# Kernel optimization log

Hardware: AMD Instinct MI355X
Metric: run time of the kernel (lower is better)

## Reference

```python
import jax, jax.numpy as jnp
import numpy as np

D_IN = 512
HLS = [1024, 1024, 512]
N_Q = 4096
N_K = 16384
N_CLASSES = 100
BN_EPS = 1e-5


def _bn(x, gamma, beta):
    # BatchNorm1d in training mode: per-batch mean/biased-var normalization
    m = jnp.mean(x, axis=0)
    v = jnp.var(x, axis=0)
    return gamma * (x - m) * jax.lax.rsqrt(v + BN_EPS) + beta


def _neg_cdist(a, b):
    # -||a_i - b_j||_2 via expanded form (GEMM-dominated)
    a2 = jnp.sum(a * a, axis=1, keepdims=True)          # [N,1]
    b2 = jnp.sum(b * b, axis=1, keepdims=True).T        # [1,M]
    d2 = a2 + b2 - 2.0 * (a @ b.T)                      # [N,M]
    return -jnp.sqrt(jnp.maximum(d2, 0.0))


def setup_inputs() -> dict:
    key = jax.random.key(0)
    ks = jax.random.split(key, 32)
    inp = {
        "x": jax.random.normal(ks[0], (N_Q, D_IN), jnp.float32),
        "x_n": jax.random.normal(ks[1], (N_K, D_IN), jnp.float32),
        "y_n": jax.random.randint(ks[2], (N_K,), 0, N_CLASSES, jnp.int32),
        "in_gamma": jnp.ones((D_IN,), jnp.float32),
        "in_beta": jnp.zeros((D_IN,), jnp.float32),
    }
    dims = [D_IN] + HLS
    ki = 3
    for i in range(len(HLS)):
        fan_in = dims[i]
        bound = 1.0 / np.sqrt(fan_in)
        inp[f"W{i}"] = jax.random.uniform(ks[ki], (dims[i + 1], dims[i]), jnp.float32, -bound, bound); ki += 1
        inp[f"b{i}"] = jax.random.uniform(ks[ki], (dims[i + 1],), jnp.float32, -bound, bound); ki += 1
        inp[f"g{i}"] = jnp.ones((dims[i + 1],), jnp.float32)
        inp[f"bt{i}"] = jnp.zeros((dims[i + 1],), jnp.float32)
    return inp


def reference(x, x_n, y_n, in_gamma, in_beta,
              W0, b0, g0, bt0, W1, b1, g1, bt1, W2, b2, g2, bt2):
    x = _bn(x, in_gamma, in_beta)
    x_n = _bn(x_n, in_gamma, in_beta)
    layers = [(W0, b0, g0, bt0), (W1, b1, g1, bt1), (W2, b2, g2, bt2)]
    for W, b, g, bt in layers:
        x = _bn(jnp.tanh(x @ W.T + b), g, bt)
        x_n = _bn(jnp.tanh(x_n @ W.T + b), g, bt)
    sim = _neg_cdist(x, x_n)                       # [N_Q, N_K]
    scores = jax.nn.softmax(sim, axis=1)
    y_ohe = jax.nn.one_hot(y_n, N_CLASSES, dtype=x.dtype)  # [N_K, C]
    return jnp.clip(scores @ y_ohe, 0.0, 1.0)
```

## Files before the change

### kernel.cpp

```cpp
#include <hip/hip_runtime.h>
#include <math.h>

#define NQ 4096
#define NK 16384
#define NROWS 20480
#define NCLS 100
#define PCLS 112
#define DCH 16

typedef __attribute__((ext_vector_type(8))) short bf16x8;
typedef __attribute__((ext_vector_type(4))) float f32x4;

__device__ inline unsigned short f2bf(float f) {
  unsigned u = __float_as_uint(f);
  u += 0x7fff + ((u >> 16) & 1);
  return (unsigned short)(u >> 16);
}
__device__ inline void upk(unsigned u, float& a, float& b) {
  a = __uint_as_float(u << 16);
  b = __uint_as_float(u & 0xffff0000u);
}
__device__ inline float fast_tanh(float x) {
  float e = __expf(2.f * x);
  return 1.f - 2.f / (e + 1.f);
}
__device__ inline void gload_lds16(const unsigned short* g, unsigned short* l) {
  __builtin_amdgcn_global_load_lds(
      (const __attribute__((address_space(1))) unsigned int*)g,
      (__attribute__((address_space(3))) unsigned int*)l, 16, 0, 0);
}

__global__ __launch_bounds__(256) void conv2_bf16(
    const float* __restrict__ x, const float* __restrict__ xn,
    unsigned short* __restrict__ outp) {
  const size_t n4q = (size_t)NQ * 512 / 4;
  const size_t n4 = (size_t)NROWS * 512 / 4;
  size_t i = (size_t)blockIdx.x * 256 + threadIdx.x;
  size_t stride = (size_t)gridDim.x * 256;
  for (; i < n4; i += stride) {
    float4 v = (i < n4q) ? ((const float4*)x)[i] : ((const float4*)xn)[i - n4q];
    unsigned lo = (unsigned)f2bf(v.x) | ((unsigned)f2bf(v.y) << 16);
    unsigned hi = (unsigned)f2bf(v.z) | ((unsigned)f2bf(v.w) << 16);
    ((uint2*)outp)[i] = make_uint2(lo, hi);
  }
}

__global__ __launch_bounds__(256) void colstats2(
    const float* __restrict__ x, const float* __restrict__ xn,
    float* __restrict__ part) {
  int j = blockIdx.x * 256 + threadIdx.x;
  int c = blockIdx.y;
  int seg = blockIdx.z;
  const float* A = seg ? xn : x;
  int rpc = seg ? (NK / 64) : (NQ / 64);
  float* p4 = part + (size_t)seg * 64 * 2 * 512;
  const float* p = A + (size_t)c * rpc * 512 + j;
  float s = 0.f, s2 = 0.f;
#pragma unroll 4
  for (int r = 0; r < rpc; ++r) {
    float v = p[(size_t)r * 512];
    s += v; s2 += v * v;
  }
  p4[(size_t)c * 2 * 512 + j] = s;
  p4[(size_t)c * 2 * 512 + 512 + j] = s2;
}

__global__ __launch_bounds__(256) void finish_ab2(
    const float* __restrict__ part,
    const float* __restrict__ g, const float* __restrict__ bt,
    float* __restrict__ abq, float* __restrict__ abk) {
  int j = blockIdx.x * 256 + threadIdx.x;
  int seg = blockIdx.y;
  const float* p4 = part + (size_t)seg * 64 * 2 * 512;
  float invN = seg ? (1.0f / NK) : (1.0f / NQ);
  float* ab = seg ? abk : abq;
  float s = 0.f, s2 = 0.f;
  for (int c = 0; c < 64; ++c) {
    s += p4[(size_t)c * 2 * 512 + j];
    s2 += p4[(size_t)c * 2 * 512 + 512 + j];
  }
  float m = s * invN;
  float v = fmaxf(s2 * invN - m * m, 0.f);
  float a = g[j] * rsqrtf(v + 1e-5f);
  ab[2 * j] = a;
  ab[2 * j + 1] = bt[j] - a * m;
}

__global__ __launch_bounds__(256) void ab_from_stats2(
    const float* __restrict__ stq, const float* __restrict__ stk,
    const float* __restrict__ g, const float* __restrict__ bt,
    float* __restrict__ abq, float* __restrict__ abk, int M) {
  int j = blockIdx.x * 256 + threadIdx.x;
  if (j >= M) return;
  int seg = blockIdx.y;
  const float* st = seg ? stk : stq;
  float invN = seg ? (1.0f / NK) : (1.0f / NQ);
  float* ab = seg ? abk : abq;
  float s = st[2 * j], s2 = st[2 * j + 1];
  float m = s * invN;
  float v = fmaxf(s2 * invN - m * m, 0.f);
  float a = g[j] * rsqrtf(v + 1e-5f);
  ab[2 * j] = a;
  ab[2 * j + 1] = bt[j] - a * m;
}

__global__ __launch_bounds__(256) void fold_w2(
    const float* __restrict__ W, const float* __restrict__ b,
    const float* __restrict__ abq, const float* __restrict__ abk, int K,
    unsigned short* __restrict__ Woq, unsigned short* __restrict__ Wok,
    float* __restrict__ boq, float* __restrict__ bok,
    float* __restrict__ statq, float* __restrict__ statk, int M) {
  int j = blockIdx.x;
  int t = threadIdx.x;
  if (j == 0) for (int i = t; i < 2 * M; i += 256) statq[i] = 0.f;
  if (j == 1) for (int i = t; i < 2 * M; i += 256) statk[i] = 0.f;
  const float* Wr = W + (size_t)j * K;
  unsigned short* Wq = Woq + (size_t)j * K;
  unsigned short* Wk = Wok + (size_t)j * K;
  float sq = 0.f, sk = 0.f;
  for (int k = t; k < K; k += 256) {
    float w = Wr[k];
    Wq[k] = f2bf(abq[2 * k] * w);
    Wk[k] = f2bf(abk[2 * k] * w);
    sq += abq[2 * k + 1] * w;
    sk += abk[2 * k + 1] * w;
  }
  __shared__ float redq[4], redk[4];
#pragma unroll
  for (int off = 32; off; off >>= 1) {
    sq += __shfl_down(sq, off, 64);
    sk += __shfl_down(sk, off, 64);
  }
  if ((t & 63) == 0) { redq[t >> 6] = sq; redk[t >> 6] = sk; }
  __syncthreads();
  if (t == 0) {
    boq[j] = b[j] + redq[0] + redq[1] + redq[2] + redq[3];
    bok[j] = b[j] + redk[0] + redk[1] + redk[2] + redk[3];
  }
}

__global__ __launch_bounds__(256) void gemm_v8(
    const unsigned short* __restrict__ A,
    const unsigned short* __restrict__ Wq, const unsigned short* __restrict__ Wk,
    const float* __restrict__ bq, const float* __restrict__ bk,
    unsigned short* __restrict__ C,
    float* __restrict__ stq, float* __restrict__ stk, int M, int K) {
  __shared__ unsigned short As[4][128 * 32];
  __shared__ unsigned short Ws[4][128 * 32];
  int tid = threadIdx.x;
  int l = tid & 63, w = tid >> 6;
  int rowBase = blockIdx.y * 128, colBase = blockIdx.x * 128;
  int seg = rowBase >= NQ;
  const unsigned short* W = seg ? Wk : Wq;
  const float* bias = seg ? bk : bq;
  float* st = seg ? stk : stq;
  int rowOff = (w >> 1) * 64, colOff = (w & 1) * 64;
  int fr = l & 15, fc = l >> 4;

  const unsigned short* Ag[2];
  const unsigned short* Wg[2];
  int slot[2];
#pragma unroll
  for (int j = 0; j < 2; ++j) {
    int i = tid + j * 256;
    int r = i >> 2, c = (i & 3) ^ (r & 3);
    slot[j] = i * 8;
    Ag[j] = A + (size_t)(rowBase + r) * K + c * 8;
    Wg[j] = W + (size_t)(colBase + r) * K + c * 8;
  }
  auto stage = [&](int s, int bb) {
    int ko = s * 32;
#pragma unroll
    for (int j = 0; j < 2; ++j) {
      gload_lds16(Ag[j] + ko, &As[bb][0] + slot[j]);
      gload_lds16(Wg[j] + ko, &Ws[bb][0] + slot[j]);
    }
  };

  f32x4 acc[4][4];
#pragma unroll
  for (int m = 0; m < 4; ++m)
#pragma unroll
    for (int n = 0; n < 4; ++n) acc[m][n] = (f32x4){0.f, 0.f, 0.f, 0.f};

  int NS = K >> 5;
  stage(0, 0);
  stage(1, 1);
  stage(2, 2);
  for (int s = 0; s < NS; ++s) {
    if (s + 2 < NS) {
      asm volatile("s_waitcnt vmcnt(8)" ::: "memory");
    } else if (s + 1 < NS) {
      asm volatile("s_waitcnt vmcnt(4)" ::: "memory");
    } else {
      asm volatile("s_waitcnt vmcnt(0)" ::: "memory");
    }
    __builtin_amdgcn_s_barrier();
    __builtin_amdgcn_sched_barrier(0);
    int b = s & 3;
    bf16x8 av[4], bv[4];
#pragma unroll
    for (int m = 0; m < 4; ++m) {
      int row = rowOff + m * 16 + fr;
      int p = fc ^ (row & 3);
      av[m] = *(const bf16x8*)((const char*)&As[b][0] + row * 64 + p * 16);
    }
#pragma unroll
    for (int n = 0; n < 4; ++n) {
      int row = colOff + n * 16 + fr;
      int p = fc ^ (row & 3);
      bv[n] = *(const bf16x8*)((const char*)&Ws[b][0] + row * 64 + p * 16);
    }
    if (s + 3 < NS) stage(s + 3, (s + 3) & 3);
#pragma unroll
    for (int m = 0; m < 4; ++m)
#pragma unroll
      for (int n = 0; n < 4; ++n)
        acc[m][n] = __builtin_amdgcn_mfma_f32_16x16x32_bf16(av[m], bv[n], acc[m][n], 0, 0, 0);
  }

  float ts1[4] = {0.f, 0.f, 0.f, 0.f};
  float ts2[4] = {0.f, 0.f, 0.f, 0.f};
#pragma unroll
  for (int m = 0; m < 4; ++m) {
#pragma unroll
    for (int r = 0; r < 4; ++r) {
      size_t row = rowBase + rowOff + m * 16 + fc * 4 + r;
      unsigned short* Crow = C + row * M;
#pragma unroll
      for (int n = 0; n < 4; ++n) {
        int col = colBase + colOff + n * 16 + fr;
        float val = fast_tanh(acc[m][n][r] + bias[col]);
        Crow[col] = f2bf(val);
        ts1[n] += val;
        ts2[n] += val * val;
      }
    }
  }
#pragma unroll
  for (int n = 0; n < 4; ++n) {
    float s1 = ts1[n], s2 = ts2[n];
    s1 += __shfl_xor(s1, 16, 64); s1 += __shfl_xor(s1, 32, 64);
    s2 += __shfl_xor(s2, 16, 64); s2 += __shfl_xor(s2, 32, 64);
    if (fc == 0) {
      int col = colBase + colOff + n * 16 + fr;
      atomicAdd(&st[2 * col], s1);
      atomicAdd(&st[2 * col + 1], s2);
    }
  }
}

__global__ __launch_bounds__(256) void bn_final2(
    unsigned short* __restrict__ F, const float* __restrict__ abq,
    const float* __restrict__ abk, float* __restrict__ norms) {
  int w = threadIdx.x >> 6, l = threadIdx.x & 63;
  int row = blockIdx.x * 4 + w;
  const float* ab = (row < NQ) ? abq : abk;
  unsigned short* p = F + (size_t)row * 512 + l * 8;
  uint4 v = *(const uint4*)p;
  int j0 = l * 8;
  float f[8];
  upk(v.x, f[0], f[1]); upk(v.y, f[2], f[3]);
  upk(v.z, f[4], f[5]); upk(v.w, f[6], f[7]);
  float s = 0.f;
  unsigned pk[4];
#pragma unroll
  for (int e = 0; e < 8; e += 2) {
    float a0 = ab[2 * (j0 + e)] * f[e] + ab[2 * (j0 + e) + 1];
    float a1 = ab[2 * (j0 + e + 1)] * f[e + 1] + ab[2 * (j0 + e + 1) + 1];
    s += a0 * a0 + a1 * a1;
    pk[e >> 1] = (unsigned)f2bf(a0) | ((unsigned)f2bf(a1) << 16);
  }
  *(uint4*)p = make_uint4(pk[0], pk[1], pk[2], pk[3]);
#pragma unroll
  for (int off = 32; off; off >>= 1) s += __shfl_down(s, off, 64);
  if (l == 0) norms[row] = s;
}

__global__ __launch_bounds__(256) void scatter_ohe(
    const int* __restrict__ yn, unsigned short* __restrict__ oheT) {
  int k = blockIdx.x * 256 + threadIdx.x;
  if (k < NK) oheT[(size_t)yn[k] * NK + k] = 0x3F80;
}

__global__ __launch_bounds__(512, 2) void dist_v5(
    const unsigned short* __restrict__ F,
    const float* __restrict__ norms,
    const unsigned short* __restrict__ oheT,
    float* __restrict__ part) {
  __shared__ unsigned short kbuf[3][128 * 64];
  __shared__ unsigned short Qs[8 * 64 * 64];
  __shared__ unsigned short Ps[64][136];
  __shared__ float k2s[1024];
  int tid = threadIdx.x;
  int l = tid & 63, w = tid >> 6;
  int qBase = blockIdx.x * 64;
  int kBase0 = blockIdx.y * 1024;
  int mg = w & 1, ng = w >> 1;
  int qtw = w & 3, cth = w >> 2;
  int fr = l & 15, fc = l >> 4;

  for (int i = tid; i < 1024; i += 512) k2s[i] = norms[NQ + kBase0 + i];
  float q2r0 = norms[qBase + mg * 32 + fr];
  float q2r1 = norms[qBase + mg * 32 + 16 + fr];
  __builtin_amdgcn_sched_barrier(0);

#pragma unroll
  for (int j = 0; j < 8; ++j) {
    int i = tid + j * 512;
    int ss = i >> 9;
    int row = (i >> 3) & 63;
    int c = (i & 7) ^ (row & 7);
    gload_lds16(F + (size_t)(qBase + row) * 512 + ss * 64 + c * 8, Qs + i * 8);
  }

  int i0 = tid, i1 = tid + 512;
  int r0 = i0 >> 3, c0 = (i0 & 7) ^ (r0 & 7);
  int r1 = i1 >> 3, c1 = (i1 & 7) ^ (r1 & 7);
  auto stage = [&](int slice, int bb) {
    int kRow = kBase0 + (slice >> 3) * 128;
    int ko = (slice & 7) * 64;
    gload_lds16(F + (size_t)(NQ + kRow + r0) * 512 + ko + c0 * 8,
                &kbuf[bb][0] + i0 * 8);
    gload_lds16(F + (size_t)(NQ + kRow + r1) * 512 + ko + c1 * 8,
                &kbuf[bb][0] + i1 * 8);
  };

  f32x4 accC[4];
#pragma unroll
  for (int c = 0; c < 4; ++c) accC[c] = (f32x4){0.f, 0.f, 0.f, 0.f};

  stage(0, 0);
  stage(1, 1);
  asm volatile("s_waitcnt lgkmcnt(0)" ::: "memory");

  for (int kt = 0; kt < 8; ++kt) {
    f32x4 acc[2][2];
#pragma unroll
    for (int t2 = 0; t2 < 2; ++t2)
#pragma unroll
      for (int qt = 0; qt < 2; ++qt) acc[t2][qt] = (f32x4){0.f, 0.f, 0.f, 0.f};
    bf16x8 ob[4][4];
#pragma unroll
    for (int kc = 0; kc < 4; ++kc)
#pragma unroll
      for (int c = 0; c < 4; ++c) ob[kc][c] = (bf16x8){0, 0, 0, 0, 0, 0, 0, 0};
#pragma unroll
    for (int s = 0; s < 8; ++s) {
      int slice = kt * 8 + s;
      if (slice == 63) {
        asm volatile("s_waitcnt vmcnt(0)" ::: "memory");
      } else if (s == 1 || s == 2) {
        asm volatile("s_waitcnt vmcnt(18)" ::: "memory");
      } else {
        asm volatile("s_waitcnt vmcnt(2)" ::: "memory");
      }
      __builtin_amdgcn_s_barrier();
      __builtin_amdgcn_sched_barrier(0);
      int b = slice % 3;
      bf16x8 kv[2][2];
#pragma unroll
      for (int kc = 0; kc < 2; ++kc)
#pragma unroll
        for (int t2 = 0; t2 < 2; ++t2) {
          int row = ng * 32 + t2 * 16 + fr;
          int sl = (kc * 4 + fc) ^ (row & 7);
          kv[kc][t2] = *(const bf16x8*)((const char*)&kbuf[b][0] + row * 128 + sl * 16);
        }
      bf16x8 avx[2][2];
#pragma unroll
      for (int kc = 0; kc < 2; ++kc)
#pragma unroll
        for (int qt = 0; qt < 2; ++qt) {
          int row = mg * 32 + qt * 16 + fr;
          int sl = (kc * 4 + fc) ^ (fr & 7);
          avx[kc][qt] = *(const bf16x8*)((const char*)Qs + s * 8192 + row * 128 + sl * 16);
        }
      if (slice + 2 < 64) stage(slice + 2, (slice + 2) % 3);
      if (s == 0) {
        __builtin_amdgcn_sched_barrier(0);
#pragma unroll
        for (int kc = 0; kc < 4; ++kc)
#pragma unroll
          for (int c = 0; c < 4; ++c) {
            int ctg = cth * 4 + c;
            if (ctg < 7)
              ob[kc][c] = *(const bf16x8*)(
                  oheT + (size_t)(ctg * 16 + fr) * NK + kBase0 + kt * 128 + kc * 32 + fc * 8);
          }
        __builtin_amdgcn_sched_barrier(0);
      }
#pragma unroll
      for (int kc = 0; kc < 2; ++kc)
#pragma unroll
        for (int t2 = 0; t2 < 2; ++t2)
#pragma unroll
          for (int qt = 0; qt < 2; ++qt)
            acc[t2][qt] = __builtin_amdgcn_mfma_f32_16x16x32_bf16(
                kv[kc][t2], avx[kc][qt], acc[t2][qt], 0, 0, 0);
    }
#pragma unroll
    for (int t2 = 0; t2 < 2; ++t2) {
      float k2v[4];
#pragma unroll
      for (int r = 0; r < 4; ++r)
        k2v[r] = k2s[kt * 128 + ng * 32 + t2 * 16 + fc * 4 + r];
#pragma unroll
      for (int qt = 0; qt < 2; ++qt) {
        int q = mg * 32 + qt * 16 + fr;
        float q2 = qt ? q2r1 : q2r0;
        float pv[4];
#pragma unroll
        for (int r = 0; r < 4; ++r) {
          float d2 = q2 + k2v[r] - 2.f * acc[t2][qt][r];
          pv[r] = __expf(-sqrtf(fmaxf(d2, 0.f)));
        }
        unsigned lo = (unsigned)f2bf(pv[0]) | ((unsigned)f2bf(pv[1]) << 16);
        unsigned hi = (unsigned)f2bf(pv[2]) | ((unsigned)f2bf(pv[3]) << 16);
        *(uint2*)(&Ps[q][ng * 32 + t2 * 16 + fc * 4]) = make_uint2(lo, hi);
      }
    }
    asm volatile("s_waitcnt lgkmcnt(0)" ::: "memory");
    __builtin_amdgcn_s_barrier();
    __builtin_amdgcn_sched_barrier(0);
#pragma unroll
    for (int kc = 0; kc < 4; ++kc) {
      bf16x8 pa = *(const bf16x8*)(&Ps[qtw * 16 + fr][kc * 32 + fc * 8]);
#pragma unroll
      for (int c = 0; c < 4; ++c) {
        int ctg = cth * 4 + c;
        if (ctg < 7)
          accC[c] = __builtin_amdgcn_mfma_f32_16x16x32_bf16(pa, ob[kc][c], accC[c], 0, 0, 0);
      }
    }
  }
#pragma unroll
  for (int c = 0; c < 4; ++c) {
    int ctg = cth * 4 + c;
    if (ctg < 7) {
#pragma unroll
      for (int r = 0; r < 4; ++r) {
        int q = qBase + qtw * 16 + fc * 4 + r;
        part[((size_t)q * DCH + blockIdx.y) * PCLS + ctg * 16 + fr] = accC[c][r];
      }
    }
  }
}

__global__ __launch_bounds__(128) void combine_out(
    const float* __restrict__ part, float* __restrict__ outp) {
  int q = blockIdx.x;
  int t = threadIdx.x;
  float num = 0.f;
  if (t < NCLS) {
#pragma unroll
    for (int ch = 0; ch < DCH; ++ch)
      num += part[((size_t)q * DCH + ch) * PCLS + t];
  }
  __shared__ float sn[128];
  sn[t] = (t < NCLS) ? num : 0.f;
  __syncthreads();
#pragma unroll
  for (int off = 64; off; off >>= 1) {
    if (t < off) sn[t] += sn[t + off];
    __syncthreads();
  }
  float L = sn[0];
  if (t < NCLS) outp[(size_t)q * NCLS + t] = fminf(fmaxf(num / L, 0.f), 1.f);
}

extern "C" void kernel_launch(void* const* d_in, const int* in_sizes, int n_in,
                              void* d_out, int out_size, void* d_ws, size_t ws_size,
                              hipStream_t stream) {
  (void)in_sizes; (void)n_in; (void)out_size; (void)ws_size;
  const float* x   = (const float*)d_in[0];
  const float* xn  = (const float*)d_in[1];
  const int*   yn  = (const int*)d_in[2];
  const float* ing = (const float*)d_in[3];
  const float* inb = (const float*)d_in[4];
  const float* Wl[3]  = {(const float*)d_in[5], (const float*)d_in[9],  (const float*)d_in[13]};
  const float* bl[3]  = {(const float*)d_in[6], (const float*)d_in[10], (const float*)d_in[14]};
  const float* gl[3]  = {(const float*)d_in[7], (const float*)d_in[11], (const float*)d_in[15]};
  const float* btl[3] = {(const float*)d_in[8], (const float*)d_in[12], (const float*)d_in[16]};
  float* outp = (float*)d_out;

  unsigned short* featA = (unsigned short*)d_ws;
  unsigned short* featB = featA + (size_t)NROWS * 1024;
  unsigned short* wq  = featB + (size_t)NROWS * 1024;
  unsigned short* wk  = wq + (size_t)1024 * 1024;
  unsigned short* ohe = wk + (size_t)1024 * 1024;
  float* spart = (float*)(ohe + (size_t)PCLS * NK);
  float* abq   = spart + 2 * 64 * 2 * 512;
  float* abk   = abq + 2048;
  float* statq = abk + 2048;
  float* statk = statq + 2048;
  float* bpq   = statk + 2048;
  float* bpk   = bpq + 1024;
  float* norms = bpk + 1024;
  float* part  = norms + NROWS;

  colstats2<<<dim3(2, 64, 2), 256, 0, stream>>>(x, xn, spart);
  finish_ab2<<<dim3(2, 2), 256, 0, stream>>>(spart, ing, inb, abq, abk);

  conv2_bf16<<<2048, 256, 0, stream>>>(x, xn, featA);

  hipMemsetAsync(ohe, 0, (size_t)PCLS * NK * sizeof(unsigned short), stream);
  scatter_ohe<<<NK / 256, 256, 0, stream>>>(yn, ohe);

  int dims[4] = {512, 1024, 1024, 512};
  unsigned short *src = featA, *dst = featB;
  for (int lyr = 0; lyr < 3; ++lyr) {
    int K = dims[lyr], M = dims[lyr + 1];
    fold_w2<<<M, 256, 0, stream>>>(Wl[lyr], bl[lyr], abq, abk, K,
                                   wq, wk, bpq, bpk, statq, statk, M);
    gemm_v8<<<dim3(M / 128, NROWS / 128), 256, 0, stream>>>(
        src, wq, wk, bpq, bpk, dst, statq, statk, M, K);
    ab_from_stats2<<<dim3((M + 255) / 256, 2), 256, 0, stream>>>(
        statq, statk, gl[lyr], btl[lyr], abq, abk, M);
    unsigned short* t = src; src = dst; dst = t;
  }
  bn_final2<<<NROWS / 4, 256, 0, stream>>>(src, abq, abk, norms);

  dist_v5<<<dim3(NQ / 64, DCH), 512, 0, stream>>>(src, norms, ohe, part);
  combine_out<<<NQ, 128, 0, stream>>>(part, outp);
}
```

Measured before the change: 503.7 us.

## Load key tiles directly from global memory into registers, dropping LDS triple buffer

The distance kernel no longer stages key-feature slices through a triple-buffered shared-memory ring with async global-to-LDS loads and per-slice barriers. Each wave now reads its key fragments straight from global memory into registers, and the one-hot class tiles are loaded unconditionally at the start of each key tile, with the class index clamped. This removes per-slice barriers and frees LDS, which may allow higher occupancy. In exchange, the global loads are uncoalesced and duplicated across the waves that share a key tile, and the loads are not software-pipelined, so memory latency may be exposed.

```diff
diff --git a/kernel.cpp b/kernel.cpp
--- a/kernel.cpp
+++ b/kernel.cpp
@@ -283,12 +283,11 @@
   if (k < NK) oheT[(size_t)yn[k] * NK + k] = 0x3F80;
 }
 
-__global__ __launch_bounds__(512, 2) void dist_v5(
+__global__ __launch_bounds__(512, 2) void dist_v10(
     const unsigned short* __restrict__ F,
     const float* __restrict__ norms,
     const unsigned short* __restrict__ oheT,
     float* __restrict__ part) {
-  __shared__ unsigned short kbuf[3][128 * 64];
   __shared__ unsigned short Qs[8 * 64 * 64];
   __shared__ unsigned short Ps[64][136];
   __shared__ float k2s[1024];
@@ -303,7 +302,6 @@
   for (int i = tid; i < 1024; i += 512) k2s[i] = norms[NQ + kBase0 + i];
   float q2r0 = norms[qBase + mg * 32 + fr];
   float q2r1 = norms[qBase + mg * 32 + 16 + fr];
-  __builtin_amdgcn_sched_barrier(0);
 
 #pragma unroll
   for (int j = 0; j < 8; ++j) {
@@ -313,26 +311,12 @@
     int c = (i & 7) ^ (row & 7);
     gload_lds16(F + (size_t)(qBase + row) * 512 + ss * 64 + c * 8, Qs + i * 8);
   }
-
-  int i0 = tid, i1 = tid + 512;
-  int r0 = i0 >> 3, c0 = (i0 & 7) ^ (r0 & 7);
-  int r1 = i1 >> 3, c1 = (i1 & 7) ^ (r1 & 7);
-  auto stage = [&](int slice, int bb) {
-    int kRow = kBase0 + (slice >> 3) * 128;
-    int ko = (slice & 7) * 64;
-    gload_lds16(F + (size_t)(NQ + kRow + r0) * 512 + ko + c0 * 8,
-                &kbuf[bb][0] + i0 * 8);
-    gload_lds16(F + (size_t)(NQ + kRow + r1) * 512 + ko + c1 * 8,
-                &kbuf[bb][0] + i1 * 8);
-  };
+  asm volatile("s_waitcnt vmcnt(0) lgkmcnt(0)" ::: "memory");
+  __builtin_amdgcn_s_barrier();
 
   f32x4 accC[4];
 #pragma unroll
   for (int c = 0; c < 4; ++c) accC[c] = (f32x4){0.f, 0.f, 0.f, 0.f};
-
-  stage(0, 0);
-  stage(1, 1);
-  asm volatile("s_waitcnt lgkmcnt(0)" ::: "memory");
 
   for (int kt = 0; kt < 8; ++kt) {
     f32x4 acc[2][2];
@@ -344,29 +328,22 @@
 #pragma unroll
     for (int kc = 0; kc < 4; ++kc)
 #pragma unroll
-      for (int c = 0; c < 4; ++c) ob[kc][c] = (bf16x8){0, 0, 0, 0, 0, 0, 0, 0};
+      for (int c = 0; c < 4; ++c) {
+        int ctg = cth * 4 + c;
+        int ctgl = ctg < 7 ? ctg : 6;
+        ob[kc][c] = *(const bf16x8*)(
+            oheT + (size_t)(ctgl * 16 + fr) * NK + kBase0 + kt * 128 + kc * 32 + fc * 8);
+      }
+    const unsigned short* kb0 =
+        F + (size_t)(NQ + kBase0 + kt * 128 + ng * 32 + fr) * 512 + fc * 8;
 #pragma unroll
     for (int s = 0; s < 8; ++s) {
-      int slice = kt * 8 + s;
-      if (slice == 63) {
-        asm volatile("s_waitcnt vmcnt(0)" ::: "memory");
-      } else if (s == 1 || s == 2) {
-        asm volatile("s_waitcnt vmcnt(18)" ::: "memory");
-      } else {
-        asm volatile("s_waitcnt vmcnt(2)" ::: "memory");
-      }
-      __builtin_amdgcn_s_barrier();
-      __builtin_amdgcn_sched_barrier(0);
-      int b = slice % 3;
       bf16x8 kv[2][2];
 #pragma unroll
       for (int kc = 0; kc < 2; ++kc)
 #pragma unroll
-        for (int t2 = 0; t2 < 2; ++t2) {
-          int row = ng * 32 + t2 * 16 + fr;
-          int sl = (kc * 4 + fc) ^ (row & 7);
-          kv[kc][t2] = *(const bf16x8*)((const char*)&kbuf[b][0] + row * 128 + sl * 16);
-        }
+        for (int t2 = 0; t2 < 2; ++t2)
+          kv[kc][t2] = *(const bf16x8*)(kb0 + (size_t)t2 * 16 * 512 + s * 64 + kc * 32);
       bf16x8 avx[2][2];
 #pragma unroll
       for (int kc = 0; kc < 2; ++kc)
@@ -376,20 +353,6 @@
           int sl = (kc * 4 + fc) ^ (fr & 7);
           avx[kc][qt] = *(const bf16x8*)((const char*)Qs + s * 8192 + row * 128 + sl * 16);
         }
-      if (slice + 2 < 64) stage(slice + 2, (slice + 2) % 3);
-      if (s == 0) {
-        __builtin_amdgcn_sched_barrier(0);
-#pragma unroll
-        for (int kc = 0; kc < 4; ++kc)
-#pragma unroll
-          for (int c = 0; c < 4; ++c) {
-            int ctg = cth * 4 + c;
-            if (ctg < 7)
-              ob[kc][c] = *(const bf16x8*)(
-                  oheT + (size_t)(ctg * 16 + fr) * NK + kBase0 + kt * 128 + kc * 32 + fc * 8);
-          }
-        __builtin_amdgcn_sched_barrier(0);
-      }
 #pragma unroll
       for (int kc = 0; kc < 2; ++kc)
 #pragma unroll
@@ -399,6 +362,7 @@
             acc[t2][qt] = __builtin_amdgcn_mfma_f32_16x16x32_bf16(
                 kv[kc][t2], avx[kc][qt], acc[t2][qt], 0, 0, 0);
     }
+    __builtin_amdgcn_s_barrier();
 #pragma unroll
     for (int t2 = 0; t2 < 2; ++t2) {
       float k2v[4];
@@ -422,7 +386,6 @@
     }
     asm volatile("s_waitcnt lgkmcnt(0)" ::: "memory");
     __builtin_amdgcn_s_barrier();
-    __builtin_amdgcn_sched_barrier(0);
 #pragma unroll
     for (int kc = 0; kc < 4; ++kc) {
       bf16x8 pa = *(const bf16x8*)(&Ps[qtw * 16 + fr][kc * 32 + fc * 8]);
@@ -521,6 +484,6 @@
   }
   bn_final2<<<NROWS / 4, 256, 0, stream>>>(src, abq, abk, norms);
 
-  dist_v5<<<dim3(NQ / 64, DCH), 512, 0, stream>>>(src, norms, ohe, part);
+  dist_v10<<<dim3(NQ / 64, DCH), 512, 0, stream>>>(src, norms, ohe, part);
   combine_out<<<NQ, 128, 0, stream>>>(part, outp);
 }
```

Result: slower. 669.4 us (+32.9%).

## Fold BN stats finalization into weight folding and remap GEMM blocks across XCDs

Applied to the files above, without the earlier changes.

Removes the per-layer ab_from_stats2 launch by computing the BatchNorm scale/shift directly from the previous layer's accumulated statistics inside fold_w2, using ping-pong stat buffers so zeroing the current buffer does not clobber the one being read. A single ab_from_stats2 call remains for the final layer. Separately, gemm_v8 remaps its linear block index so consecutive blocks on the same XCD share row tiles, aiming for better L2 reuse of A. The fold kernel now redoes the rsqrt per output row, a small amount of redundant work.

```diff
diff --git a/kernel.cpp b/kernel.cpp
--- a/kernel.cpp
+++ b/kernel.cpp
@@ -106,24 +106,44 @@
 
 __global__ __launch_bounds__(256) void fold_w2(
     const float* __restrict__ W, const float* __restrict__ b,
-    const float* __restrict__ abq, const float* __restrict__ abk, int K,
+    const float* __restrict__ abq, const float* __restrict__ abk,
+    const float* __restrict__ stq, const float* __restrict__ stk,
+    const float* __restrict__ g, const float* __restrict__ bt,
+    int K,
     unsigned short* __restrict__ Woq, unsigned short* __restrict__ Wok,
     float* __restrict__ boq, float* __restrict__ bok,
-    float* __restrict__ statq, float* __restrict__ statk, int M) {
+    float* __restrict__ statzq, float* __restrict__ statzk, int M,
+    int useStats) {
   int j = blockIdx.x;
   int t = threadIdx.x;
-  if (j == 0) for (int i = t; i < 2 * M; i += 256) statq[i] = 0.f;
-  if (j == 1) for (int i = t; i < 2 * M; i += 256) statk[i] = 0.f;
+  if (j == 0) for (int i = t; i < 2 * M; i += 256) statzq[i] = 0.f;
+  if (j == 1) for (int i = t; i < 2 * M; i += 256) statzk[i] = 0.f;
   const float* Wr = W + (size_t)j * K;
   unsigned short* Wq = Woq + (size_t)j * K;
   unsigned short* Wk = Wok + (size_t)j * K;
   float sq = 0.f, sk = 0.f;
   for (int k = t; k < K; k += 256) {
     float w = Wr[k];
-    Wq[k] = f2bf(abq[2 * k] * w);
-    Wk[k] = f2bf(abk[2 * k] * w);
-    sq += abq[2 * k + 1] * w;
-    sk += abk[2 * k + 1] * w;
+    float aq, bq_, ak, bk_;
+    if (useStats) {
+      float s = stq[2 * k], s2 = stq[2 * k + 1];
+      float m = s * (1.0f / NQ);
+      float v = fmaxf(s2 * (1.0f / NQ) - m * m, 0.f);
+      aq = g[k] * rsqrtf(v + 1e-5f);
+      bq_ = bt[k] - aq * m;
+      s = stk[2 * k]; s2 = stk[2 * k + 1];
+      m = s * (1.0f / NK);
+      v = fmaxf(s2 * (1.0f / NK) - m * m, 0.f);
+      ak = g[k] * rsqrtf(v + 1e-5f);
+      bk_ = bt[k] - ak * m;
+    } else {
+      aq = abq[2 * k]; bq_ = abq[2 * k + 1];
+      ak = abk[2 * k]; bk_ = abk[2 * k + 1];
+    }
+    Wq[k] = f2bf(aq * w);
+    Wk[k] = f2bf(ak * w);
+    sq += bq_ * w;
+    sk += bk_ * w;
   }
   __shared__ float redq[4], redk[4];
 #pragma unroll
@@ -149,7 +169,12 @@
   __shared__ unsigned short Ws[4][128 * 32];
   int tid = threadIdx.x;
   int l = tid & 63, w = tid >> 6;
-  int rowBase = blockIdx.y * 128, colBase = blockIdx.x * 128;
+  int nx = gridDim.x;
+  int lin = blockIdx.y * nx + blockIdx.x;
+  int xcd = lin & 7, j = lin >> 3;
+  int rowB = (j / nx) * 8 + xcd;
+  int colB = j % nx;
+  int rowBase = rowB * 128, colBase = colB * 128;
   int seg = rowBase >= NQ;
   const unsigned short* W = seg ? Wk : Wq;
   const float* bias = seg ? bk : bq;
@@ -161,19 +186,19 @@
   const unsigned short* Wg[2];
   int slot[2];
 #pragma unroll
-  for (int j = 0; j < 2; ++j) {
-    int i = tid + j * 256;
+  for (int jj = 0; jj < 2; ++jj) {
+    int i = tid + jj * 256;
     int r = i >> 2, c = (i & 3) ^ (r & 3);
-    slot[j] = i * 8;
-    Ag[j] = A + (size_t)(rowBase + r) * K + c * 8;
-    Wg[j] = W + (size_t)(colBase + r) * K + c * 8;
+    slot[jj] = i * 8;
+    Ag[jj] = A + (size_t)(rowBase + r) * K + c * 8;
+    Wg[jj] = W + (size_t)(colBase + r) * K + c * 8;
   }
   auto stage = [&](int s, int bb) {
     int ko = s * 32;
 #pragma unroll
-    for (int j = 0; j < 2; ++j) {
-      gload_lds16(Ag[j] + ko, &As[bb][0] + slot[j]);
-      gload_lds16(Wg[j] + ko, &Ws[bb][0] + slot[j]);
+    for (int jj = 0; jj < 2; ++jj) {
+      gload_lds16(Ag[jj] + ko, &As[bb][0] + slot[jj]);
+      gload_lds16(Wg[jj] + ko, &Ws[bb][0] + slot[jj]);
     }
   };
 
@@ -492,9 +517,11 @@
   float* spart = (float*)(ohe + (size_t)PCLS * NK);
   float* abq   = spart + 2 * 64 * 2 * 512;
   float* abk   = abq + 2048;
-  float* statq = abk + 2048;
-  float* statk = statq + 2048;
-  float* bpq   = statk + 2048;
+  float* stAq  = abk + 2048;
+  float* stAk  = stAq + 2048;
+  float* stBq  = stAk + 2048;
+  float* stBk  = stBq + 2048;
+  float* bpq   = stBk + 2048;
   float* bpk   = bpq + 1024;
   float* norms = bpk + 1024;
   float* part  = norms + NROWS;
@@ -511,14 +538,20 @@
   unsigned short *src = featA, *dst = featB;
   for (int lyr = 0; lyr < 3; ++lyr) {
     int K = dims[lyr], M = dims[lyr + 1];
-    fold_w2<<<M, 256, 0, stream>>>(Wl[lyr], bl[lyr], abq, abk, K,
-                                   wq, wk, bpq, bpk, statq, statk, M);
+    float* curQ = (lyr & 1) ? stBq : stAq;
+    float* curK = (lyr & 1) ? stBk : stAk;
+    float* prevQ = (lyr & 1) ? stAq : stBq;
+    float* prevK = (lyr & 1) ? stAk : stBk;
+    fold_w2<<<M, 256, 0, stream>>>(
+        Wl[lyr], bl[lyr], abq, abk, prevQ, prevK,
+        lyr ? gl[lyr - 1] : ing, lyr ? btl[lyr - 1] : inb,
+        K, wq, wk, bpq, bpk, curQ, curK, M, lyr > 0);
     gemm_v8<<<dim3(M / 128, NROWS / 128), 256, 0, stream>>>(
-        src, wq, wk, bpq, bpk, dst, statq, statk, M, K);
-    ab_from_stats2<<<dim3((M + 255) / 256, 2), 256, 0, stream>>>(
-        statq, statk, gl[lyr], btl[lyr], abq, abk, M);
+        src, wq, wk, bpq, bpk, dst, curQ, curK, M, K);
     unsigned short* t = src; src = dst; dst = t;
   }
+  ab_from_stats2<<<dim3(2, 2), 256, 0, stream>>>(
+      stAq, stAk, gl[2], btl[2], abq, abk, 512);
   bn_final2<<<NROWS / 4, 256, 0, stream>>>(src, abq, abk, norms);
 
   dist_v5<<<dim3(NQ / 64, DCH), 512, 0, stream>>>(src, norms, ohe, part);
```

New measurement: 480.8 us. 1.05x faster.
